# Kernel optimization log

Measured on AMD Instinct MI355X. Metric: run time of the kernel, lower is better.

Reference implementation:

```python
import jax, jax.numpy as jnp
import numpy as np

HIDDEN = 1024
B, S = 4, 2048


def setup_inputs() -> dict:
    key = jax.random.key(0)
    ks = jax.random.split(key, 9)
    scale = 1.0 / np.sqrt(HIDDEN)
    mk = lambda k: (jax.random.normal(k, (HIDDEN, HIDDEN), dtype=jnp.float32) * scale)
    return {
        "x": jax.random.normal(ks[0], (B, S, HIDDEN), dtype=jnp.float32),
        "Wq": mk(ks[1]), "bq": jnp.zeros((HIDDEN,), jnp.float32),
        "Wk": mk(ks[2]), "bk": jnp.zeros((HIDDEN,), jnp.float32),
        "Wv": mk(ks[3]), "bv": jnp.zeros((HIDDEN,), jnp.float32),
        "Wo": mk(ks[4]), "bo": jnp.zeros((HIDDEN,), jnp.float32),
    }


def reference(x, Wq, bq, Wk, bk, Wv, bv, Wo, bo):
    # Single-head attention over the full hidden dim (num_heads unused in source).
    # Linear(H,H): y = x @ W^T + b ; weights stored [out,in] torch-style.
    q = jnp.einsum("bsh,oh->bso", x, Wq) + bq  # [B,S,H]
    k = jnp.einsum("bsh,oh->bso", x, Wk) + bk
    v = jnp.einsum("bsh,oh->bso", x, Wv) + bv
    scores = jnp.einsum("bqh,bkh->bqk", q, k) / jnp.sqrt(jnp.float32(HIDDEN))
    attn = jax.nn.softmax(scores, axis=-1)  # dropout rate is 0.0 (eval-equivalent)
    ctx = jnp.einsum("bqk,bkh->bqh", attn, v)
    return jnp.einsum("bsh,oh->bso", ctx, Wo) + bo
```

## Files before the change

### kernel.cpp

```cpp
#include <hip/hip_runtime.h>

#define HID 1024
#define SEQ 2048
#define NB 4
#define BS 8192

typedef __attribute__((ext_vector_type(8))) short short8;
typedef __attribute__((ext_vector_type(8))) unsigned short ushort8;
typedef __attribute__((ext_vector_type(4))) float f32x4;

__device__ __forceinline__ float bf2f(unsigned short u) {
  unsigned int x = ((unsigned int)u) << 16;
  return __builtin_bit_cast(float, x);
}
__device__ __forceinline__ unsigned short f2bf(float f) {
  unsigned int x = __builtin_bit_cast(unsigned int, f);
  x = x + 0x7fffu + ((x >> 16) & 1u);
  return (unsigned short)(x >> 16);
}

#define GLOAD16(g, l)                                                          \
  __builtin_amdgcn_global_load_lds(                                            \
      (const __attribute__((address_space(1))) unsigned int*)(g),              \
      (__attribute__((address_space(3))) unsigned int*)(l), 16, 0, 0)

__global__ void cast_f32_to_bf16(const float* __restrict__ in,
                                 unsigned short* __restrict__ out, int n) {
  int i = (blockIdx.x * 256 + threadIdx.x) * 8;
  if (i >= n) return;
  f32x4 a = *(const f32x4*)(in + i);
  f32x4 b = *(const f32x4*)(in + i + 4);
  ushort8 o;
  o[0] = f2bf(a[0]); o[1] = f2bf(a[1]); o[2] = f2bf(a[2]); o[3] = f2bf(a[3]);
  o[4] = f2bf(b[0]); o[5] = f2bf(b[1]); o[6] = f2bf(b[2]); o[7] = f2bf(b[3]);
  *(ushort8*)(out + i) = o;
}

__global__ __launch_bounds__(256) void transpose_cast(
    const float* __restrict__ in, unsigned short* __restrict__ out) {
  __shared__ float t[32][33];
  const int bx = blockIdx.x * 32, by = blockIdx.y * 32;
  const int tx = threadIdx.x & 31, ty = threadIdx.x >> 5;
#pragma unroll
  for (int i = 0; i < 4; ++i)
    t[ty + i * 8][tx] = in[(by + ty + i * 8) * 1024 + bx + tx];
  __syncthreads();
#pragma unroll
  for (int i = 0; i < 4; ++i)
    out[(bx + ty + i * 8) * 1024 + by + tx] = f2bf(t[tx][ty + i * 8]);
}

__global__ __launch_bounds__(256) void bias_fuse(const float* __restrict__ Wo,
                                                 const float* __restrict__ bv,
                                                 const float* __restrict__ bo,
                                                 float* __restrict__ bp) {
  const int row = blockIdx.x * 4 + (threadIdx.x >> 6);
  const int lane = threadIdx.x & 63;
  float s = 0.f;
  for (int k = lane; k < 1024; k += 64) s += Wo[row * 1024 + k] * bv[k];
#pragma unroll
  for (int off = 32; off >= 1; off >>= 1) s += __shfl_xor(s, off, 64);
  if (lane == 0) bp[row] = s + bo[row];
}

template <int BN, int OUT_F32, int BIAS_MODE, int EPI>
__global__ __launch_bounds__(256, (BN == 128 ? 3 : 4)) void gemm_b(
    const unsigned short* __restrict__ A, const unsigned short* __restrict__ B,
    void* __restrict__ Cv, const float* __restrict__ bias,
    const float* __restrict__ bias2, float* __restrict__ Srow, int K, int lda,
    int ldb, int ldc, long long bsA, long long bsB, long long bsC,
    float alpha) {
  static_assert(BN == 128 || BN == 64, "BN");
  constexpr int NF = BN / 32;

  __shared__ unsigned short lA[2][128 * 32];
  __shared__ unsigned short lB[2][BN * 32];

  const int tid = threadIdx.x;
  const int lane = tid & 63, wid = tid >> 6;
  const int fr = lane & 15, fq = lane >> 4;
  const int wm = wid >> 1, wn = wid & 1;

  const int nx = gridDim.x;
  const int nwg = nx * gridDim.y;
  int f = blockIdx.y * nx + blockIdx.x;
  f = (f & 7) * (nwg >> 3) + (f >> 3);
  const int bx = f % nx, by = f / nx;
  const int bz = blockIdx.z;

  const unsigned short* Ag = A + bz * bsA + (long long)by * 128 * lda;
  const unsigned short* Bg = B + bz * bsB + (long long)bx * BN * ldb;
  const int NT = K >> 5;

  const int srow = tid >> 2;
  const int scol = 8 * ((tid & 3) ^ ((tid >> 3) & 3));
  const int lbase = wid * 512;

  auto stageA = [&](int t, int b) {
    unsigned short* d = &lA[b][lbase];
    GLOAD16(Ag + (long long)srow * lda + t * 32 + scol, d);
    GLOAD16(Ag + (long long)(64 + srow) * lda + t * 32 + scol, d + 2048);
  };
  auto stageB = [&](int t, int b) {
    unsigned short* d = &lB[b][lbase];
    GLOAD16(Bg + (long long)srow * ldb + t * 32 + scol, d);
    if (BN == 128)
      GLOAD16(Bg + (long long)(64 + srow) * ldb + t * 32 + scol, d + 2048);
  };

  const int xm = ((fr >> 1) & 3) << 3;

  f32x4 acc[4][NF] = {};

  auto compute = [&](const unsigned short* pa, const unsigned short* pb) {
    short8 av[4], bw[NF];
#pragma unroll
    for (int i = 0; i < 4; ++i)
      av[i] = *(const short8*)(pa +
                               (((wm * 64 + i * 16 + fr) * 32 + fq * 8) ^ xm));
#pragma unroll
    for (int n = 0; n < NF; ++n)
      bw[n] = *(const short8*)(pb + (((wn * (BN / 2) + n * 16 + fr) * 32 +
                                      fq * 8) ^ xm));
    asm volatile("s_waitcnt lgkmcnt(0)" ::: "memory");
    __builtin_amdgcn_sched_barrier(0);
#pragma unroll
    for (int i = 0; i < 4; ++i)
#pragma unroll
      for (int n = 0; n < NF; ++n)
        acc[i][n] = __builtin_amdgcn_mfma_f32_16x16x32_bf16(av[i], bw[n],
                                                            acc[i][n], 0, 0, 0);
  };

  stageA(0, 0);
  stageB(0, 0);
  __syncthreads();

  for (int t = 0; t < NT; t += 2) {
    stageA(t + 1, 1);
    stageB(t + 1, 1);
    compute(lA[0], lB[0]);
    __syncthreads();
    if (t + 2 < NT) {
      stageA(t + 2, 0);
      stageB(t + 2, 0);
    }
    compute(lA[1], lB[1]);
    __syncthreads();
  }

  const long long cb0 = (long long)bz * bsC;
  float* sredf = (float*)lA;
#pragma unroll
  for (int i = 0; i < 4; ++i)
#pragma unroll
    for (int j = 0; j < 4; ++j) {
      const int row = wm * 64 + i * 16 + fq * 4 + j;
      float inv = 1.0f;
      if (EPI == 2) inv = 1.0f / Srow[(long long)bz * SEQ + by * 128 + row];
      float rps = 0.0f;
#pragma unroll
      for (int n = 0; n < NF; ++n) {
        const int col = bx * BN + wn * (BN / 2) + n * 16 + fr;
        float v = acc[i][n][j] * alpha;
        if (EPI == 1) { v = __expf(v); rps += v; }
        if (EPI == 2) v *= inv;
        if (BIAS_MODE == 1) v += bias[col];
        if (BIAS_MODE == 3) v += (col < 1024) ? bias[col] : bias2[col - 1024];
        const long long idx = cb0 + (long long)(by * 128 + row) * ldc + col;
        if (OUT_F32)
          ((float*)Cv)[idx] = v;
        else
          ((unsigned short*)Cv)[idx] = f2bf(v);
      }
      if (EPI == 1) {
        rps += __shfl_xor(rps, 1, 64);
        rps += __shfl_xor(rps, 2, 64);
        rps += __shfl_xor(rps, 4, 64);
        rps += __shfl_xor(rps, 8, 64);
        if (fr == 0) sredf[row * 2 + wn] = rps;
      }
    }
  if (EPI == 1) {
    __syncthreads();
    if (tid < 128) {
      const float s2 = sredf[tid * 2] + sredf[tid * 2 + 1];
      atomicAdd(Srow + (long long)bz * SEQ + by * 128 + tid, s2);
    }
  }
}

extern "C" void kernel_launch(void* const* d_in, const int* in_sizes, int n_in,
                              void* d_out, int out_size, void* d_ws,
                              size_t ws_size, hipStream_t stream) {
  (void)in_sizes; (void)n_in; (void)out_size; (void)ws_size;
  const float* x = (const float*)d_in[0];
  const float* Wq = (const float*)d_in[1];
  const float* bq = (const float*)d_in[2];
  const float* Wk = (const float*)d_in[3];
  const float* bk = (const float*)d_in[4];
  const float* Wv = (const float*)d_in[5];
  const float* bv = (const float*)d_in[6];
  const float* Wo = (const float*)d_in[7];
  const float* bo = (const float*)d_in[8];
  float* out = (float*)d_out;

  char* ws = (char*)d_ws;
  unsigned short* xbf  = (unsigned short*)(ws + 0);
  unsigned short* wqk  = (unsigned short*)(ws + 16777216);
  unsigned short* wobf = (unsigned short*)(ws + 20971520);
  unsigned short* wvT  = (unsigned short*)(ws + 23068672);
  unsigned short* wov  = (unsigned short*)(ws + 25165824);
  float*          bpr  = (float*)        (ws + 27262976);
  float*          Srow = (float*)        (ws + 28311552);
  unsigned short* VWoT = (unsigned short*)(ws + 33554432);
  unsigned short* QKb  = (unsigned short*)(ws + 50331648);
  unsigned short* P    = (unsigned short*)(ws + 83886080);

  cast_f32_to_bf16<<<4096, 256, 0, stream>>>(x, xbf, BS * HID);
  cast_f32_to_bf16<<<512, 256, 0, stream>>>(Wq, wqk, HID * HID);
  cast_f32_to_bf16<<<512, 256, 0, stream>>>(Wk, wqk + HID * HID, HID * HID);
  cast_f32_to_bf16<<<512, 256, 0, stream>>>(Wo, wobf, HID * HID);
  transpose_cast<<<dim3(32, 32), 256, 0, stream>>>(Wv, wvT);
  bias_fuse<<<256, 256, 0, stream>>>(Wo, bv, bo, bpr);
  hipMemsetAsync(Srow, 0, NB * SEQ * sizeof(float), stream);

  gemm_b<128, 0, 0, 0><<<dim3(8, 8, 1), 256, 0, stream>>>(
      wobf, wvT, wov, nullptr, nullptr, nullptr, HID, HID, HID, HID, 0, 0, 0,
      1.0f);
  gemm_b<64, 0, 0, 0><<<dim3(128, 8, 1), 256, 0, stream>>>(
      wov, xbf, VWoT, nullptr, nullptr, nullptr, HID, HID, HID, BS, 0, 0, 0,
      1.0f);
  gemm_b<128, 0, 3, 0><<<dim3(16, 64, 1), 256, 0, stream>>>(
      xbf, wqk, QKb, bq, bk, nullptr, HID, HID, HID, 2048, 0, 0, 0, 1.0f);
  gemm_b<128, 0, 0, 1><<<dim3(16, 16, NB), 256, 0, stream>>>(
      QKb, QKb + 1024, P, nullptr, nullptr, Srow, HID, 2048, 2048, SEQ,
      (long long)SEQ * 2048, (long long)SEQ * 2048, (long long)SEQ * SEQ,
      0.03125f);
  gemm_b<64, 1, 1, 2><<<dim3(16, 16, NB), 256, 0, stream>>>(
      P, VWoT, out, bpr, nullptr, Srow, SEQ, SEQ, BS, HID,
      (long long)SEQ * SEQ, (long long)SEQ, (long long)SEQ * HID, 1.0f);
}
```

Measured before the change: 245.0 us.

## Fold Wq and Wk into one Gram matrix to shrink QK projection

Precomputes G = Wq^T·Wk so scores become (x·G)·x^T plus a per-key bias vector. Query-only bias terms are dropped because they are constant along each softmax row. This halves the projection GEMM work and removes the strided QK buffer. It also unifies all GEMMs on a 128-wide tile and drops the explicit LDS wait/sched barrier. The trade-off is extra small kernels and an additional bf16 rounding of G.

```diff
diff --git a/kernel.cpp b/kernel.cpp
--- a/kernel.cpp
+++ b/kernel.cpp
@@ -63,18 +63,49 @@
   if (lane == 0) bp[row] = s + bo[row];
 }
 
-template <int BN, int OUT_F32, int BIAS_MODE, int EPI>
-__global__ __launch_bounds__(256, (BN == 128 ? 3 : 4)) void gemm_b(
+__global__ __launch_bounds__(256) void col_gemv(const float* __restrict__ W,
+                                                const float* __restrict__ b,
+                                                float* __restrict__ out) {
+  const int a = blockIdx.x * 256 + threadIdx.x;
+  float s = 0.f;
+  for (int h = 0; h < 1024; ++h) s += W[h * 1024 + a] * b[h];
+  out[a] = s;
+}
+
+__global__ void dot_bias(const float* __restrict__ bq,
+                         const float* __restrict__ bk, float* __restrict__ c) {
+  __shared__ float red[4];
+  const int tid = threadIdx.x;
+  float s = 0.f;
+  for (int i = tid; i < 1024; i += 256) s += bq[i] * bk[i];
+#pragma unroll
+  for (int o = 32; o >= 1; o >>= 1) s += __shfl_xor(s, o, 64);
+  if ((tid & 63) == 0) red[tid >> 6] = s;
+  __syncthreads();
+  if (tid == 0) c[0] = red[0] + red[1] + red[2] + red[3];
+}
+
+__global__ __launch_bounds__(256) void row_gemv_cb(const float* __restrict__ x,
+                                                   const float* __restrict__ v,
+                                                   const float* __restrict__ c,
+                                                   float* __restrict__ cb) {
+  const int j = blockIdx.x * 4 + (threadIdx.x >> 6);
+  const int lane = threadIdx.x & 63;
+  float s = 0.f;
+  for (int a = lane; a < 1024; a += 64) s += x[(long long)j * 1024 + a] * v[a];
+#pragma unroll
+  for (int o = 32; o >= 1; o >>= 1) s += __shfl_xor(s, o, 64);
+  if (lane == 0) cb[j] = (s + c[0]) * 0.03125f;
+}
+
+template <int OUT_F32, int BIAS_MODE, int EPI>
+__global__ __launch_bounds__(256, 3) void gemm_tlp(
     const unsigned short* __restrict__ A, const unsigned short* __restrict__ B,
     void* __restrict__ Cv, const float* __restrict__ bias,
-    const float* __restrict__ bias2, float* __restrict__ Srow, int K, int lda,
-    int ldb, int ldc, long long bsA, long long bsB, long long bsC,
-    float alpha) {
-  static_assert(BN == 128 || BN == 64, "BN");
-  constexpr int NF = BN / 32;
-
+    float* __restrict__ Srow, int K, int lda, int ldb, int ldc, long long bsA,
+    long long bsB, long long bsC, float alpha) {
   __shared__ unsigned short lA[2][128 * 32];
-  __shared__ unsigned short lB[2][BN * 32];
+  __shared__ unsigned short lB[2][128 * 32];
 
   const int tid = threadIdx.x;
   const int lane = tid & 63, wid = tid >> 6;
@@ -89,7 +120,7 @@
   const int bz = blockIdx.z;
 
   const unsigned short* Ag = A + bz * bsA + (long long)by * 128 * lda;
-  const unsigned short* Bg = B + bz * bsB + (long long)bx * BN * ldb;
+  const unsigned short* Bg = B + bz * bsB + (long long)bx * 128 * ldb;
   const int NT = K >> 5;
 
   const int srow = tid >> 2;
@@ -104,30 +135,27 @@
   auto stageB = [&](int t, int b) {
     unsigned short* d = &lB[b][lbase];
     GLOAD16(Bg + (long long)srow * ldb + t * 32 + scol, d);
-    if (BN == 128)
-      GLOAD16(Bg + (long long)(64 + srow) * ldb + t * 32 + scol, d + 2048);
+    GLOAD16(Bg + (long long)(64 + srow) * ldb + t * 32 + scol, d + 2048);
   };
 
   const int xm = ((fr >> 1) & 3) << 3;
 
-  f32x4 acc[4][NF] = {};
+  f32x4 acc[4][4] = {};
 
   auto compute = [&](const unsigned short* pa, const unsigned short* pb) {
-    short8 av[4], bw[NF];
+    short8 av[4], bw[4];
 #pragma unroll
     for (int i = 0; i < 4; ++i)
       av[i] = *(const short8*)(pa +
                                (((wm * 64 + i * 16 + fr) * 32 + fq * 8) ^ xm));
 #pragma unroll
-    for (int n = 0; n < NF; ++n)
-      bw[n] = *(const short8*)(pb + (((wn * (BN / 2) + n * 16 + fr) * 32 +
-                                      fq * 8) ^ xm));
-    asm volatile("s_waitcnt lgkmcnt(0)" ::: "memory");
-    __builtin_amdgcn_sched_barrier(0);
+    for (int n = 0; n < 4; ++n)
+      bw[n] = *(const short8*)(pb +
+                               (((wn * 64 + n * 16 + fr) * 32 + fq * 8) ^ xm));
 #pragma unroll
     for (int i = 0; i < 4; ++i)
 #pragma unroll
-      for (int n = 0; n < NF; ++n)
+      for (int n = 0; n < 4; ++n)
         acc[i][n] = __builtin_amdgcn_mfma_f32_16x16x32_bf16(av[i], bw[n],
                                                             acc[i][n], 0, 0, 0);
   };
@@ -160,13 +188,13 @@
       if (EPI == 2) inv = 1.0f / Srow[(long long)bz * SEQ + by * 128 + row];
       float rps = 0.0f;
 #pragma unroll
-      for (int n = 0; n < NF; ++n) {
-        const int col = bx * BN + wn * (BN / 2) + n * 16 + fr;
+      for (int n = 0; n < 4; ++n) {
+        const int col = bx * 128 + wn * 64 + n * 16 + fr;
         float v = acc[i][n][j] * alpha;
-        if (EPI == 1) { v = __expf(v); rps += v; }
         if (EPI == 2) v *= inv;
         if (BIAS_MODE == 1) v += bias[col];
-        if (BIAS_MODE == 3) v += (col < 1024) ? bias[col] : bias2[col - 1024];
+        if (BIAS_MODE == 4) v += bias[(long long)bz * SEQ + col];
+        if (EPI == 1) { v = __expf(v); rps += v; }
         const long long idx = cb0 + (long long)(by * 128 + row) * ldc + col;
         if (OUT_F32)
           ((float*)Cv)[idx] = v;
@@ -207,37 +235,44 @@
 
   char* ws = (char*)d_ws;
   unsigned short* xbf  = (unsigned short*)(ws + 0);
-  unsigned short* wqk  = (unsigned short*)(ws + 16777216);
-  unsigned short* wobf = (unsigned short*)(ws + 20971520);
-  unsigned short* wvT  = (unsigned short*)(ws + 23068672);
-  unsigned short* wov  = (unsigned short*)(ws + 25165824);
-  float*          bpr  = (float*)        (ws + 27262976);
-  float*          Srow = (float*)        (ws + 28311552);
-  unsigned short* VWoT = (unsigned short*)(ws + 33554432);
-  unsigned short* QKb  = (unsigned short*)(ws + 50331648);
-  unsigned short* P    = (unsigned short*)(ws + 83886080);
+  unsigned short* WqT  = (unsigned short*)(ws + 16777216);
+  unsigned short* WkT  = (unsigned short*)(ws + 18874368);
+  unsigned short* wvT  = (unsigned short*)(ws + 20971520);
+  unsigned short* wobf = (unsigned short*)(ws + 23068672);
+  unsigned short* GT   = (unsigned short*)(ws + 25165824);
+  unsigned short* wov  = (unsigned short*)(ws + 27262976);
+  float*          bpr  = (float*)        (ws + 29360128);
+  float*          vvec = (float*)        (ws + 29425664);
+  float*          cdot = (float*)        (ws + 29491200);
+  float*          cb   = (float*)        (ws + 29556736);
+  float*          Srow = (float*)        (ws + 29622272);
+  unsigned short* U    = (unsigned short*)(ws + 33554432);
+  unsigned short* VWoT = (unsigned short*)(ws + 50331648);
+  unsigned short* P    = (unsigned short*)(ws + 67108864);
 
   cast_f32_to_bf16<<<4096, 256, 0, stream>>>(x, xbf, BS * HID);
-  cast_f32_to_bf16<<<512, 256, 0, stream>>>(Wq, wqk, HID * HID);
-  cast_f32_to_bf16<<<512, 256, 0, stream>>>(Wk, wqk + HID * HID, HID * HID);
+  transpose_cast<<<dim3(32, 32), 256, 0, stream>>>(Wq, WqT);
+  transpose_cast<<<dim3(32, 32), 256, 0, stream>>>(Wk, WkT);
+  transpose_cast<<<dim3(32, 32), 256, 0, stream>>>(Wv, wvT);
   cast_f32_to_bf16<<<512, 256, 0, stream>>>(Wo, wobf, HID * HID);
-  transpose_cast<<<dim3(32, 32), 256, 0, stream>>>(Wv, wvT);
   bias_fuse<<<256, 256, 0, stream>>>(Wo, bv, bo, bpr);
+  col_gemv<<<4, 256, 0, stream>>>(Wk, bq, vvec);
+  dot_bias<<<1, 256, 0, stream>>>(bq, bk, cdot);
   hipMemsetAsync(Srow, 0, NB * SEQ * sizeof(float), stream);
 
-  gemm_b<128, 0, 0, 0><<<dim3(8, 8, 1), 256, 0, stream>>>(
-      wobf, wvT, wov, nullptr, nullptr, nullptr, HID, HID, HID, HID, 0, 0, 0,
-      1.0f);
-  gemm_b<64, 0, 0, 0><<<dim3(128, 8, 1), 256, 0, stream>>>(
-      wov, xbf, VWoT, nullptr, nullptr, nullptr, HID, HID, HID, BS, 0, 0, 0,
-      1.0f);
-  gemm_b<128, 0, 3, 0><<<dim3(16, 64, 1), 256, 0, stream>>>(
-      xbf, wqk, QKb, bq, bk, nullptr, HID, HID, HID, 2048, 0, 0, 0, 1.0f);
-  gemm_b<128, 0, 0, 1><<<dim3(16, 16, NB), 256, 0, stream>>>(
-      QKb, QKb + 1024, P, nullptr, nullptr, Srow, HID, 2048, 2048, SEQ,
-      (long long)SEQ * 2048, (long long)SEQ * 2048, (long long)SEQ * SEQ,
-      0.03125f);
-  gemm_b<64, 1, 1, 2><<<dim3(16, 16, NB), 256, 0, stream>>>(
-      P, VWoT, out, bpr, nullptr, Srow, SEQ, SEQ, BS, HID,
-      (long long)SEQ * SEQ, (long long)SEQ, (long long)SEQ * HID, 1.0f);
-}
+  gemm_tlp<0, 0, 0><<<dim3(8, 8, 1), 256, 0, stream>>>(
+      WkT, WqT, GT, nullptr, nullptr, HID, HID, HID, HID, 0, 0, 0, 1.0f);
+  gemm_tlp<0, 0, 0><<<dim3(8, 8, 1), 256, 0, stream>>>(
+      wobf, wvT, wov, nullptr, nullptr, HID, HID, HID, HID, 0, 0, 0, 1.0f);
+  gemm_tlp<0, 0, 0><<<dim3(8, 64, 1), 256, 0, stream>>>(
+      xbf, GT, U, nullptr, nullptr, HID, HID, HID, HID, 0, 0, 0, 1.0f);
+  row_gemv_cb<<<2048, 256, 0, stream>>>(x, vvec, cdot, cb);
+  gemm_tlp<0, 0, 0><<<dim3(64, 8, 1), 256, 0, stream>>>(
+      wov, xbf, VWoT, nullptr, nullptr, HID, HID, HID, BS, 0, 0, 0, 1.0f);
+  gemm_tlp<0, 4, 1><<<dim3(16, 16, NB), 256, 0, stream>>>(
+      U, xbf, P, cb, Srow, HID, HID, HID, SEQ, (long long)SEQ * HID,
+      (long long)SEQ * HID, (long long)SEQ * SEQ, 0.03125f);
+  gemm_tlp<1, 1, 2><<<dim3(8, 16, NB), 256, 0, stream>>>(
+      P, VWoT, out, bpr, Srow, SEQ, SEQ, BS, HID, (long long)SEQ * SEQ,
+      (long long)SEQ, (long long)SEQ * HID, 1.0f);
+}
```

After: 291.3 us. 18.9% more time.
